# Kernel optimization log

Hardware: AMD Instinct MI355X
Metric: run time of the kernel (lower is better)

The kernel has to match this reference:

```python
import jax, jax.numpy as jnp
import numpy as np

N = 131072
F_IN = 256
FEATURES = 64
N_SOURCES = 32


def setup_inputs() -> dict:
    key = jax.random.key(0)
    k1, k2, k3 = jax.random.split(key, 3)
    x = jax.random.normal(k1, (N, F_IN), dtype=jnp.float32)
    source = jax.random.randint(k2, (N,), 0, N_SOURCES, dtype=jnp.int32)
    W = jax.random.normal(k3, (F_IN, N_SOURCES * FEATURES), dtype=jnp.float32) * (1.0 / np.sqrt(F_IN))
    b = jnp.zeros((N_SOURCES * FEATURES,), dtype=jnp.float32)
    return {"x": x, "source": source, "W": W, "b": b}


def reference(x, source, W, b):
    # Dense projection to all sources: (N, n_sources*features)
    y = jnp.dot(x, W) + b
    # Per-row gather of the slice belonging to this row's source id.
    # Equivalent to y[i, source[i]*FEATURES : (source[i]+1)*FEATURES].
    y = y.reshape(x.shape[0], N_SOURCES, FEATURES)
    out = jnp.take_along_axis(y, source[:, None, None].astype(jnp.int32), axis=1)
    return out[:, 0, :]  # (N, FEATURES)
```

## Files before the change

kernel.cpp:

```cpp
#include <hip/hip_runtime.h>

#define N_ROWS   131072
#define F_IN     256
#define FEAT     64
#define NSRC     32
#define WSTRIDE  (NSRC * FEAT)
#define NCH      16
#define CHUNK    8192
#define LCAP     640
#define NBUCK    (NCH * NSRC)
#define KPAD     264
#define RSTRIDE  260
#define BUFF     (16 * RSTRIDE)
#define POOLF    (8 * BUFF)

#define MCHUNK   4096
#define LCAP1    512

typedef __attribute__((ext_vector_type(8))) short  bf16x8;
typedef __attribute__((ext_vector_type(4))) float  f32x4;

__device__ __forceinline__ unsigned short f2bf(float f) {
    union { float f; unsigned u; } c; c.f = f;
    unsigned r = c.u + 0x7fffu + ((c.u >> 16) & 1u);
    return (unsigned short)(r >> 16);
}

__device__ __forceinline__ bf16x8 pack8(f32x4 f0, f32x4 f1) {
    bf16x8 a;
    a[0] = (short)f2bf(f0[0]); a[1] = (short)f2bf(f0[1]);
    a[2] = (short)f2bf(f0[2]); a[3] = (short)f2bf(f0[3]);
    a[4] = (short)f2bf(f1[0]); a[5] = (short)f2bf(f1[1]);
    a[6] = (short)f2bf(f1[2]); a[7] = (short)f2bf(f1[3]);
    return a;
}

__device__ __forceinline__ void stage16(const float* __restrict__ x, int vr,
                                        float* buf, int lane) {
    #pragma unroll
    for (int r = 0; r < 16; ++r) {
        const int row = __builtin_amdgcn_readlane(vr, r);
        const float* g = x + (size_t)row * F_IN + lane * 4;
        __builtin_amdgcn_global_load_lds(
            (const __attribute__((address_space(1))) void*)g,
            (__attribute__((address_space(3))) void*)(buf + r * RSTRIDE),
            16, 0, 0);
    }
}

__global__ void zero_counts(int* __restrict__ ws) {
    const int i = blockIdx.x * 256 + threadIdx.x;
    if (i < NBUCK) ws[i] = 0;
}

__global__ __launch_bounds__(256)
void compact_kernel(const int* __restrict__ src, int* __restrict__ ws) {
    __shared__ int lcnt[NSRC];
    __shared__ int gbase[NSRC];
    const int tid = threadIdx.x;
    if (tid < NSRC) lcnt[tid] = 0;
    __syncthreads();

    const int row = blockIdx.x * 256 + tid;
    const int s   = src[row];
    const int c   = (blockIdx.x * 256) >> 13;
    const int p   = atomicAdd(&lcnt[s], 1);
    __syncthreads();
    if (tid < NSRC && lcnt[tid] > 0)
        gbase[tid] = atomicAdd(&ws[c * NSRC + tid], lcnt[tid]);
    __syncthreads();
    const int pos = gbase[s] + p;
    if (pos < LCAP)
        ws[NBUCK + ((size_t)(c * NSRC + s)) * LCAP + pos] = row;
}

__global__ __launch_bounds__(256, 1)
void gemm_kernel(const float* __restrict__ x, const float* __restrict__ W,
                 const float* __restrict__ b, const int* __restrict__ ws,
                 float* __restrict__ out) {
    __shared__ __align__(16) float pool[POOLF];
    __shared__ int lst[LCAP];

    const int tid    = threadIdx.x;
    const int c      = blockIdx.x;
    const int s      = blockIdx.y;
    const int bucket = c * NSRC + s;
    const int count  = min(ws[bucket], LCAP);
    if (count == 0) return;

    const int* gl = ws + NBUCK + (size_t)bucket * LCAP;
    for (int i = tid; i < count; i += 256) lst[i] = gl[i];

    unsigned short* Wt = (unsigned short*)pool;
    {
        const int n  = tid & 63;
        const int kp = (tid >> 6) * 2;
        #pragma unroll
        for (int k0 = 0; k0 < F_IN; k0 += 8) {
            const int k = k0 + kp;
            const float w0 = W[(size_t)k       * WSTRIDE + s * FEAT + n];
            const float w1 = W[(size_t)(k + 1) * WSTRIDE + s * FEAT + n];
            *(unsigned*)&Wt[n * KPAD + k] = (unsigned)f2bf(w0) | ((unsigned)f2bf(w1) << 16);
        }
    }
    __syncthreads();

    const int lane = tid & 63, w = tid >> 6;
    const int col  = lane & 15, quad = lane >> 4;

    bf16x8 bfrag[4][8];
    #pragma unroll
    for (int nt = 0; nt < 4; ++nt)
        #pragma unroll
        for (int kk = 0; kk < 8; ++kk)
            bfrag[nt][kk] = *(const bf16x8*)&Wt[(nt * 16 + col) * KPAD + kk * 32 + quad * 8];

    float bias[4];
    #pragma unroll
    for (int nt = 0; nt < 4; ++nt) bias[nt] = b[s * FEAT + nt * 16 + col];

    __syncthreads();

    const int ntt = (count + 15) >> 4;
    const int ntw = (w < ntt) ? (((ntt - 1 - w) >> 2) + 1) : 0;
    if (ntw == 0) return;

    float* buf0 = pool + w * (2 * BUFF);
    float* buf1 = buf0 + BUFF;

    __builtin_amdgcn_s_waitcnt(0x0F70);

    int vr_cur = lst[min(w * 16 + col, count - 1)];
    stage16(x, vr_cur, buf0, lane);

    for (int i = 0; i < ntw; ++i) {
        const int t    = w + 4 * i;
        float*    bufc = (i & 1) ? buf1 : buf0;
        const bool has_next = (i + 1 < ntw);
        const bool has_prev = (i > 0);
        int vr_next = 0;
        if (has_next) {
            vr_next = lst[min((t + 4) * 16 + col, count - 1)];
            stage16(x, vr_next, (i & 1) ? buf0 : buf1, lane);
        }
        if (has_prev && has_next)      __builtin_amdgcn_s_waitcnt(0x8F70);
        else if (has_prev || has_next) __builtin_amdgcn_s_waitcnt(0x4F70);
        else                           __builtin_amdgcn_s_waitcnt(0x0F70);

        f32x4 acc[4];
        #pragma unroll
        for (int nt = 0; nt < 4; ++nt) acc[nt] = (f32x4){0.f, 0.f, 0.f, 0.f};

        #pragma unroll
        for (int kk = 0; kk < 8; ++kk) {
            const float* ap = bufc + col * RSTRIDE + kk * 32 + quad * 8;
            const f32x4 a0 = *(const f32x4*)ap;
            const f32x4 a1 = *(const f32x4*)(ap + 4);
            const bf16x8 a = pack8(a0, a1);
            #pragma unroll
            for (int nt = 0; nt < 4; ++nt)
                acc[nt] = __builtin_amdgcn_mfma_f32_16x16x32_bf16(a, bfrag[nt][kk], acc[nt], 0, 0, 0);
        }

        #pragma unroll
        for (int nt = 0; nt < 4; ++nt)
            #pragma unroll
            for (int reg = 0; reg < 4; ++reg)
                bufc[(quad * 4 + reg) * 65 + nt * 16 + col] = acc[nt][reg] + bias[nt];
        #pragma unroll
        for (int r = 0; r < 16; ++r) {
            const int gi = t * 16 + r;
            if (gi < count) {
                const int row = __builtin_amdgcn_readlane(vr_cur, r);
                out[(size_t)row * FEAT + lane] = bufc[r * 65 + lane];
            }
        }
        vr_cur = vr_next;
    }
}

__global__ __launch_bounds__(256, 4)
void mono_kernel(const float* __restrict__ x, const int* __restrict__ src,
                 const float* __restrict__ W, const float* __restrict__ b,
                 float* __restrict__ out) {
    __shared__ __align__(16) unsigned short Wt[FEAT][KPAD];
    __shared__ int lst[LCAP1];
    __shared__ int cnt;
    const int tid = threadIdx.x, s = blockIdx.y, chunk0 = blockIdx.x * MCHUNK;
    if (tid == 0) cnt = 0;
    __syncthreads();
    {
        const int n = tid & 63, kp = (tid >> 6) * 2;
        #pragma unroll
        for (int k0 = 0; k0 < F_IN; k0 += 8) {
            const int k = k0 + kp;
            const float w0 = W[(size_t)k * WSTRIDE + s * FEAT + n];
            const float w1 = W[(size_t)(k + 1) * WSTRIDE + s * FEAT + n];
            *(unsigned*)&Wt[n][k] = (unsigned)f2bf(w0) | ((unsigned)f2bf(w1) << 16);
        }
    }
    #pragma unroll
    for (int r = 0; r < MCHUNK / 256; ++r) {
        const int row = chunk0 + r * 256 + tid;
        if (src[row] == s) {
            const int p = atomicAdd(&cnt, 1);
            if (p < LCAP1) lst[p] = row;
        }
    }
    __syncthreads();
    const int count = cnt;
    if (count == 0) return;
    const int lane = tid & 63, w = tid >> 6, col = lane & 15, quad = lane >> 4;
    float bias[4];
    #pragma unroll
    for (int nt = 0; nt < 4; ++nt) bias[nt] = b[s * FEAT + nt * 16 + col];
    const int npass = (count + 63) >> 6;
    for (int p = 0; p < npass; ++p) {
        const int base = p * 64 + w * 16;
        const int ia = lst[min(base + col, count - 1)];
        const float* ap = x + (size_t)ia * F_IN + quad * 8;
        f32x4 av[16];
        #pragma unroll
        for (int kk = 0; kk < 8; ++kk) {
            av[2 * kk]     = *(const f32x4*)(ap + kk * 32);
            av[2 * kk + 1] = *(const f32x4*)(ap + kk * 32 + 4);
        }
        f32x4 acc[4];
        #pragma unroll
        for (int nt = 0; nt < 4; ++nt) acc[nt] = (f32x4){0.f, 0.f, 0.f, 0.f};
        #pragma unroll
        for (int kk = 0; kk < 8; ++kk) {
            const bf16x8 a = pack8(av[2 * kk], av[2 * kk + 1]);
            #pragma unroll
            for (int nt = 0; nt < 4; ++nt) {
                const bf16x8 bb = *(const bf16x8*)&Wt[nt * 16 + col][kk * 32 + quad * 8];
                acc[nt] = __builtin_amdgcn_mfma_f32_16x16x32_bf16(a, bb, acc[nt], 0, 0, 0);
            }
        }
        #pragma unroll
        for (int reg = 0; reg < 4; ++reg) {
            const int gm = base + quad * 4 + reg;
            if (gm < count) {
                const int row = lst[gm];
                float* op = out + (size_t)row * FEAT;
                #pragma unroll
                for (int nt = 0; nt < 4; ++nt)
                    op[nt * 16 + col] = acc[nt][reg] + bias[nt];
            }
        }
    }
}

extern "C" void kernel_launch(void* const* d_in, const int* in_sizes, int n_in,
                              void* d_out, int out_size, void* d_ws, size_t ws_size,
                              hipStream_t stream) {
    const float* x   = (const float*)d_in[0];
    const int*   src = (const int*)d_in[1];
    const float* W   = (const float*)d_in[2];
    const float* b   = (const float*)d_in[3];
    float*       out = (float*)d_out;

    const size_t ws_needed = (size_t)NBUCK * (1 + LCAP) * sizeof(int);
    if (ws_size >= ws_needed) {
        int* ws = (int*)d_ws;
        zero_counts<<<dim3(2), dim3(256), 0, stream>>>(ws);
        compact_kernel<<<dim3(N_ROWS / 256), dim3(256), 0, stream>>>(src, ws);
        gemm_kernel<<<dim3(NCH, NSRC), dim3(256), 0, stream>>>(x, W, b, ws, out);
    } else {
        mono_kernel<<<dim3(N_ROWS / MCHUNK, NSRC), dim3(256), 0, stream>>>(x, src, W, b, out);
    }
}
```

Measured before the change: 222.5 us.

## Restructure gather GEMM into block-wide 32-row tiles with register-prefetched bf16 LDS staging

```diff
diff --git a/kernel.cpp b/kernel.cpp
--- a/kernel.cpp
+++ b/kernel.cpp
@@ -5,14 +5,13 @@
 #define FEAT     64
 #define NSRC     32
 #define WSTRIDE  (NSRC * FEAT)
-#define NCH      16
-#define CHUNK    8192
-#define LCAP     640
+#define NCH      32
+#define CHUNK    4096
+#define LCAP     320
 #define NBUCK    (NCH * NSRC)
 #define KPAD     264
-#define RSTRIDE  260
-#define BUFF     (16 * RSTRIDE)
-#define POOLF    (8 * BUFF)
+#define TPAD     66
+#define TR       32
 
 #define MCHUNK   4096
 #define LCAP1    512
@@ -35,19 +34,6 @@
     return a;
 }
 
-__device__ __forceinline__ void stage16(const float* __restrict__ x, int vr,
-                                        float* buf, int lane) {
-    #pragma unroll
-    for (int r = 0; r < 16; ++r) {
-        const int row = __builtin_amdgcn_readlane(vr, r);
-        const float* g = x + (size_t)row * F_IN + lane * 4;
-        __builtin_amdgcn_global_load_lds(
-            (const __attribute__((address_space(1))) void*)g,
-            (__attribute__((address_space(3))) void*)(buf + r * RSTRIDE),
-            16, 0, 0);
-    }
-}
-
 __global__ void zero_counts(int* __restrict__ ws) {
     const int i = blockIdx.x * 256 + threadIdx.x;
     if (i < NBUCK) ws[i] = 0;
@@ -60,10 +46,9 @@
     const int tid = threadIdx.x;
     if (tid < NSRC) lcnt[tid] = 0;
     __syncthreads();
-
     const int row = blockIdx.x * 256 + tid;
     const int s   = src[row];
-    const int c   = (blockIdx.x * 256) >> 13;
+    const int c   = blockIdx.x >> 4;
     const int p   = atomicAdd(&lcnt[s], 1);
     __syncthreads();
     if (tid < NSRC && lcnt[tid] > 0)
@@ -74,11 +59,68 @@
         ws[NBUCK + ((size_t)(c * NSRC + s)) * LCAP + pos] = row;
 }
 
-__global__ __launch_bounds__(256, 1)
+__device__ __forceinline__ void load_tile(const float* __restrict__ x,
+                                          const int* lst, int count, int tile,
+                                          int row8, int p, f32x4 av[8]) {
+    const int gi  = min(tile * TR + row8, count - 1);
+    const int row = lst[gi];
+    const float* rp = x + (size_t)row * F_IN + p * 4;
+    #pragma unroll
+    for (int i = 0; i < 8; ++i)
+        av[i] = *(const f32x4*)(rp + i * 32);
+}
+
+__device__ __forceinline__ void write_tile(unsigned short* XsBuf,
+                                           int row8, int p, const f32x4 av[8]) {
+    #pragma unroll
+    for (int i = 0; i < 8; ++i) {
+        unsigned lo = (unsigned)f2bf(av[i][0]) | ((unsigned)f2bf(av[i][1]) << 16);
+        unsigned hi = (unsigned)f2bf(av[i][2]) | ((unsigned)f2bf(av[i][3]) << 16);
+        unsigned* d = (unsigned*)&XsBuf[row8 * KPAD + i * 32 + p * 4];
+        d[0] = lo; d[1] = hi;
+    }
+}
+
+__device__ __forceinline__ void tile_compute(
+    const unsigned short* __restrict__ XsBuf, const unsigned short* __restrict__ Wt,
+    float* __restrict__ T, const int* __restrict__ lst,
+    float bias0, float bias1, float* __restrict__ out,
+    int tile, int count, int w, int lane, int col, int quad, int mh, int nh) {
+
+    f32x4 acc0 = (f32x4){0.f, 0.f, 0.f, 0.f};
+    f32x4 acc1 = (f32x4){0.f, 0.f, 0.f, 0.f};
+    #pragma unroll
+    for (int kk = 0; kk < 8; ++kk) {
+        const bf16x8 a = *(const bf16x8*)&XsBuf[(mh * 16 + col) * KPAD + kk * 32 + quad * 8];
+        const bf16x8 b0 = *(const bf16x8*)&Wt[(nh * 32 + col) * KPAD + kk * 32 + quad * 8];
+        const bf16x8 b1 = *(const bf16x8*)&Wt[(nh * 32 + 16 + col) * KPAD + kk * 32 + quad * 8];
+        acc0 = __builtin_amdgcn_mfma_f32_16x16x32_bf16(a, b0, acc0, 0, 0, 0);
+        acc1 = __builtin_amdgcn_mfma_f32_16x16x32_bf16(a, b1, acc1, 0, 0, 0);
+    }
+    #pragma unroll
+    for (int reg = 0; reg < 4; ++reg) {
+        T[(mh * 16 + quad * 4 + reg) * TPAD + nh * 32 + col]      = acc0[reg] + bias0;
+        T[(mh * 16 + quad * 4 + reg) * TPAD + nh * 32 + 16 + col] = acc1[reg] + bias1;
+    }
+    __syncthreads();
+    #pragma unroll
+    for (int r = 0; r < 8; ++r) {
+        const int lr = w * 8 + r;
+        const int gi = tile * TR + lr;
+        if (gi < count) {
+            const int grow = lst[gi];
+            out[(size_t)grow * FEAT + lane] = T[lr * TPAD + lane];
+        }
+    }
+}
+
+__global__ __launch_bounds__(256, 2)
 void gemm_kernel(const float* __restrict__ x, const float* __restrict__ W,
                  const float* __restrict__ b, const int* __restrict__ ws,
                  float* __restrict__ out) {
-    __shared__ __align__(16) float pool[POOLF];
+    __shared__ __align__(16) unsigned short Wt[FEAT * KPAD];
+    __shared__ __align__(16) unsigned short Xs[2][TR * KPAD];
+    __shared__ __align__(16) float T[TR * TPAD];
     __shared__ int lst[LCAP];
 
     const int tid    = threadIdx.x;
@@ -91,7 +133,6 @@
     const int* gl = ws + NBUCK + (size_t)bucket * LCAP;
     for (int i = tid; i < count; i += 256) lst[i] = gl[i];
 
-    unsigned short* Wt = (unsigned short*)pool;
     {
         const int n  = tid & 63;
         const int kp = (tid >> 6) * 2;
@@ -103,79 +144,34 @@
             *(unsigned*)&Wt[n * KPAD + k] = (unsigned)f2bf(w0) | ((unsigned)f2bf(w1) << 16);
         }
     }
-    __syncthreads();
 
     const int lane = tid & 63, w = tid >> 6;
     const int col  = lane & 15, quad = lane >> 4;
-
-    bf16x8 bfrag[4][8];
-    #pragma unroll
-    for (int nt = 0; nt < 4; ++nt)
-        #pragma unroll
-        for (int kk = 0; kk < 8; ++kk)
-            bfrag[nt][kk] = *(const bf16x8*)&Wt[(nt * 16 + col) * KPAD + kk * 32 + quad * 8];
-
-    float bias[4];
-    #pragma unroll
-    for (int nt = 0; nt < 4; ++nt) bias[nt] = b[s * FEAT + nt * 16 + col];
-
-    __syncthreads();
-
-    const int ntt = (count + 15) >> 4;
-    const int ntw = (w < ntt) ? (((ntt - 1 - w) >> 2) + 1) : 0;
-    if (ntw == 0) return;
-
-    float* buf0 = pool + w * (2 * BUFF);
-    float* buf1 = buf0 + BUFF;
-
-    __builtin_amdgcn_s_waitcnt(0x0F70);
-
-    int vr_cur = lst[min(w * 16 + col, count - 1)];
-    stage16(x, vr_cur, buf0, lane);
-
-    for (int i = 0; i < ntw; ++i) {
-        const int t    = w + 4 * i;
-        float*    bufc = (i & 1) ? buf1 : buf0;
-        const bool has_next = (i + 1 < ntw);
-        const bool has_prev = (i > 0);
-        int vr_next = 0;
-        if (has_next) {
-            vr_next = lst[min((t + 4) * 16 + col, count - 1)];
-            stage16(x, vr_next, (i & 1) ? buf0 : buf1, lane);
-        }
-        if (has_prev && has_next)      __builtin_amdgcn_s_waitcnt(0x8F70);
-        else if (has_prev || has_next) __builtin_amdgcn_s_waitcnt(0x4F70);
-        else                           __builtin_amdgcn_s_waitcnt(0x0F70);
-
-        f32x4 acc[4];
-        #pragma unroll
-        for (int nt = 0; nt < 4; ++nt) acc[nt] = (f32x4){0.f, 0.f, 0.f, 0.f};
-
-        #pragma unroll
-        for (int kk = 0; kk < 8; ++kk) {
-            const float* ap = bufc + col * RSTRIDE + kk * 32 + quad * 8;
-            const f32x4 a0 = *(const f32x4*)ap;
-            const f32x4 a1 = *(const f32x4*)(ap + 4);
-            const bf16x8 a = pack8(a0, a1);
-            #pragma unroll
-            for (int nt = 0; nt < 4; ++nt)
-                acc[nt] = __builtin_amdgcn_mfma_f32_16x16x32_bf16(a, bfrag[nt][kk], acc[nt], 0, 0, 0);
-        }
-
-        #pragma unroll
-        for (int nt = 0; nt < 4; ++nt)
-            #pragma unroll
-            for (int reg = 0; reg < 4; ++reg)
-                bufc[(quad * 4 + reg) * 65 + nt * 16 + col] = acc[nt][reg] + bias[nt];
-        #pragma unroll
-        for (int r = 0; r < 16; ++r) {
-            const int gi = t * 16 + r;
-            if (gi < count) {
-                const int row = __builtin_amdgcn_readlane(vr_cur, r);
-                out[(size_t)row * FEAT + lane] = bufc[r * 65 + lane];
-            }
-        }
-        vr_cur = vr_next;
+    const int mh   = w & 1,    nh   = w >> 1;
+    const int row8 = tid >> 3, p    = tid & 7;
+
+    const float bias0 = b[s * FEAT + nh * 32 + col];
+    const float bias1 = b[s * FEAT + nh * 32 + 16 + col];
+
+    __syncthreads();
+
+    const int ntiles = (count + TR - 1) / TR;
+    f32x4 avA[8], avB[8];
+    load_tile(x, lst, count, 0, row8, p, avA);
+
+    for (int t = 0; t < ntiles; t += 2) {
+        write_tile(Xs[0], row8, p, avA);
+        if (t + 1 < ntiles) load_tile(x, lst, count, t + 1, row8, p, avB);
+        __syncthreads();
+        tile_compute(Xs[0], Wt, T, lst, bias0, bias1, out,
+                     t, count, w, lane, col, quad, mh, nh);
+        if (t + 1 >= ntiles) break;
+
+        write_tile(Xs[1], row8, p, avB);
+        if (t + 2 < ntiles) load_tile(x, lst, count, t + 2, row8, p, avA);
+        __syncthreads();
+        tile_compute(Xs[1], Wt, T, lst, bias0, bias1, out,
+                     t + 1, count, w, lane, col, quad, mh, nh);
     }
 }
 
@@ -183,7 +179,7 @@
 void mono_kernel(const float* __restrict__ x, const int* __restrict__ src,
                  const float* __restrict__ W, const float* __restrict__ b,
                  float* __restrict__ out) {
-    __shared__ __align__(16) unsigned short Wt[FEAT][KPAD];
+    __shared__ __align__(16) unsigned short Wt[FEAT * KPAD];
     __shared__ int lst[LCAP1];
     __shared__ int cnt;
     const int tid = threadIdx.x, s = blockIdx.y, chunk0 = blockIdx.x * MCHUNK;
@@ -196,7 +192,7 @@
             const int k = k0 + kp;
             const float w0 = W[(size_t)k * WSTRIDE + s * FEAT + n];
             const float w1 = W[(size_t)(k + 1) * WSTRIDE + s * FEAT + n];
-            *(unsigned*)&Wt[n][k] = (unsigned)f2bf(w0) | ((unsigned)f2bf(w1) << 16);
+            *(unsigned*)&Wt[n * KPAD + k] = (unsigned)f2bf(w0) | ((unsigned)f2bf(w1) << 16);
         }
     }
     #pragma unroll
@@ -215,8 +211,8 @@
     #pragma unroll
     for (int nt = 0; nt < 4; ++nt) bias[nt] = b[s * FEAT + nt * 16 + col];
     const int npass = (count + 63) >> 6;
-    for (int p = 0; p < npass; ++p) {
-        const int base = p * 64 + w * 16;
+    for (int pp = 0; pp < npass; ++pp) {
+        const int base = pp * 64 + w * 16;
         const int ia = lst[min(base + col, count - 1)];
         const float* ap = x + (size_t)ia * F_IN + quad * 8;
         f32x4 av[16];
@@ -233,7 +229,7 @@
             const bf16x8 a = pack8(av[2 * kk], av[2 * kk + 1]);
             #pragma unroll
             for (int nt = 0; nt < 4; ++nt) {
-                const bf16x8 bb = *(const bf16x8*)&Wt[nt * 16 + col][kk * 32 + quad * 8];
+                const bf16x8 bb = *(const bf16x8*)&Wt[(nt * 16 + col) * KPAD + kk * 32 + quad * 8];
                 acc[nt] = __builtin_amdgcn_mfma_f32_16x16x32_bf16(a, bb, acc[nt], 0, 0, 0);
             }
         }
@@ -263,7 +259,7 @@
     const size_t ws_needed = (size_t)NBUCK * (1 + LCAP) * sizeof(int);
     if (ws_size >= ws_needed) {
         int* ws = (int*)d_ws;
-        zero_counts<<<dim3(2), dim3(256), 0, stream>>>(ws);
+        zero_counts<<<dim3(4), dim3(256), 0, stream>>>(ws);
         compact_kernel<<<dim3(N_ROWS / 256), dim3(256), 0, stream>>>(src, ws);
         gemm_kernel<<<dim3(NCH, NSRC), dim3(256), 0, stream>>>(x, W, b, ws, out);
     } else {
```

New measurement: 220.8 us. No clear change (-0.7%).
